# Kernel optimization log

Hardware: AMD Instinct MI355X
Metric: run time of the kernel (lower is better)

The kernel has to match this reference:

```python
import jax, jax.numpy as jnp
import numpy as np

IN_FEATURES = 1024
OUT_FEATURES = 1024
N = 8192

def setup_inputs() -> dict:
    key = jax.random.key(0)
    kx, kw, kb = jax.random.split(key, 3)
    x = jax.random.normal(kx, (N, IN_FEATURES), dtype=jnp.float32)
    # nn.Linear default init: U(-1/sqrt(in), 1/sqrt(in))
    bound = 1.0 / np.sqrt(IN_FEATURES)
    W = jax.random.uniform(kw, (OUT_FEATURES, IN_FEATURES), minval=-bound, maxval=bound, dtype=jnp.float32)
    b = jax.random.uniform(kb, (OUT_FEATURES,), minval=-bound, maxval=bound, dtype=jnp.float32)
    return {"x": x, "W": W, "b": b}

def reference(x, W, b):
    # h: [N, D]
    h = x @ W.T + b
    # scores: [N, N]; tanh applied to raw scores, softmax over dim=1 (rows)
    scores = jnp.tanh(h @ h.T)
    attn = jax.nn.softmax(scores, axis=1)
    out = jnp.tanh(attn @ h)
    return out
```

## Files before the change

kernel.cpp:

```cpp
#include <hip/hip_runtime.h>
#include <hip/hip_bf16.h>
#include <cstdint>
#include <cstddef>

typedef __bf16 bf16_t;
typedef __bf16 bf16x4 __attribute__((ext_vector_type(4)));
typedef __bf16 bf16x8 __attribute__((ext_vector_type(8)));
typedef float f32x4 __attribute__((ext_vector_type(4)));
typedef float f32x16 __attribute__((ext_vector_type(16)));
typedef float f32x2 __attribute__((ext_vector_type(2)));
typedef int i32x4 __attribute__((ext_vector_type(4)));
typedef int i32x8 __attribute__((ext_vector_type(8)));

#define NROWS 8192
#define DFEAT 1024
#define BK 32
#define NBLK 64
#define TILE_B (128 * BK)
#define F8TILE 8192
#define NTRI (NBLK * (NBLK + 1) / 2)

typedef __attribute__((address_space(3))) unsigned int lds_uint;
typedef __attribute__((address_space(1))) const unsigned int glb_uint;

__device__ __forceinline__ float fast_tanh(float x) {
  float e = __expf(2.0f * x);
  return 1.0f - 2.0f * __builtin_amdgcn_rcpf(e + 1.0f);
}

__device__ __forceinline__ unsigned pack_fp8x4(float a, float b, float c, float d) {
  unsigned v = 0;
  v = __builtin_amdgcn_cvt_pk_fp8_f32(a, b, v, false);
  v = __builtin_amdgcn_cvt_pk_fp8_f32(c, d, v, true);
  return v;
}

__global__ __launch_bounds__(256) void cast_kernel(const float* __restrict__ in,
                                                   bf16_t* __restrict__ out, int n4) {
  int i = blockIdx.x * 256 + threadIdx.x;
  if (i < n4) {
    float4 v = *(const float4*)(in + i * 4);
    bf16x4 o = {(bf16_t)v.x, (bf16_t)v.y, (bf16_t)v.z, (bf16_t)v.w};
    *(bf16x4*)(out + i * 4) = o;
  }
}

__device__ __forceinline__ void stage_async(const bf16_t* __restrict__ g, int ld,
                                            int row0, int k0, bf16_t* lds,
                                            int wave, int lane) {
#pragma unroll
  for (int t = 0; t < 2; ++t) {
    const int rb = (t * 4 + wave) * 16;
    const bf16_t* gp = g + (size_t)(row0 + rb + (lane >> 2)) * ld + (k0 + (lane & 3) * 8);
    __builtin_amdgcn_global_load_lds((glb_uint*)gp, (lds_uint*)(lds + rb * BK), 16, 0, 0);
  }
}

__device__ __forceinline__ void stage_f8(const uint8_t* __restrict__ g, int ld,
                                         int row0, int k0, uint8_t* lds,
                                         int wave, int lane) {
#pragma unroll
  for (int t = 0; t < 2; ++t) {
    const int rb = (t * 4 + wave) * 16;
    const uint8_t* gp = g + (size_t)(row0 + rb + (lane >> 2)) * ld + (k0 + (lane & 3) * 16);
    __builtin_amdgcn_global_load_lds((glb_uint*)gp, (lds_uint*)(lds + rb * 64), 16, 0, 0);
  }
}

__global__ __launch_bounds__(256) void gemm1_kernel(const bf16_t* __restrict__ xb,
                                                    const bf16_t* __restrict__ Wb,
                                                    const float* __restrict__ bias,
                                                    bf16_t* __restrict__ hout,
                                                    uint8_t* __restrict__ hT8) {
  __shared__ __align__(16) bf16_t smem[4 * TILE_B];
  const int tid = threadIdx.x;
  const int wave = tid >> 6, lane = tid & 63;
  const int wm = wave >> 1, wn = wave & 1;
  const int l15 = lane & 15, quad = lane >> 4;
  const int m0 = blockIdx.x * 128, n0 = blockIdx.y * 128;
  f32x4 acc[4][4] = {};
  const int NIT = DFEAT / BK;
  stage_async(xb, DFEAT, m0, 0, smem, wave, lane);
  stage_async(Wb, DFEAT, n0, 0, smem + TILE_B, wave, lane);
  __syncthreads();
  for (int it = 0; it < NIT; ++it) {
    bf16_t* lA = smem + (it & 1) * 2 * TILE_B;
    bf16_t* lB = lA + TILE_B;
    if (it + 1 < NIT) {
      bf16_t* nA = smem + ((it + 1) & 1) * 2 * TILE_B;
      stage_async(xb, DFEAT, m0, (it + 1) * BK, nA, wave, lane);
      stage_async(Wb, DFEAT, n0, (it + 1) * BK, nA + TILE_B, wave, lane);
    }
    bf16x8 a[4], b[4];
#pragma unroll
    for (int f = 0; f < 4; ++f) {
      a[f] = *(const bf16x8*)(lA + (wm * 64 + f * 16 + l15) * BK + quad * 8);
      b[f] = *(const bf16x8*)(lB + (wn * 64 + f * 16 + l15) * BK + quad * 8);
    }
#pragma unroll
    for (int i = 0; i < 4; ++i)
#pragma unroll
      for (int j = 0; j < 4; ++j)
        acc[i][j] = __builtin_amdgcn_mfma_f32_16x16x32_bf16(a[i], b[j], acc[i][j], 0, 0, 0);
    __syncthreads();
  }
#pragma unroll
  for (int i = 0; i < 4; ++i) {
    int rbase = m0 + wm * 64 + i * 16 + quad * 4;
#pragma unroll
    for (int j = 0; j < 4; ++j) {
      int col = n0 + wn * 64 + j * 16 + l15;
      float bv = bias[col];
      float hv[4];
#pragma unroll
      for (int r = 0; r < 4; ++r) hv[r] = acc[i][j][r] + bv;
#pragma unroll
      for (int r = 0; r < 4; ++r)
        hout[(size_t)(rbase + r) * DFEAT + col] = (bf16_t)hv[r];
      *(unsigned*)(hT8 + (size_t)col * NROWS + rbase) =
          pack_fp8x4(hv[0], hv[1], hv[2], hv[3]);
    }
  }
}

__global__ __launch_bounds__(256) void scores_sym_kernel(const bf16_t* __restrict__ h,
                                                         uint8_t* __restrict__ P,
                                                         float* __restrict__ lsum) {
  __shared__ __align__(16) char smem[128 * 144];
  bf16_t* lA = (bf16_t*)smem;
  bf16_t* lB = (bf16_t*)(smem + 128 * BK * 2);
  uint8_t (*mir)[144] = (uint8_t(*)[144])smem;

  const int k = (int)blockIdx.x & 7;
  const int s = (int)blockIdx.x >> 3;
  int I, J, r, c;
  if (s < 36) {
    I = J = k;
    int tt = s; r = 0;
    while (tt >= 8 - r) { tt -= 8 - r; ++r; }
    c = r + tt;
  } else {
    int e, t;
    if (s < 228) { e = 3 * k + (s - 36) / 64; t = (s - 36) & 63; }
    else { e = 24 + (k >> 1); t = ((k & 1) << 5) + (s - 228); }
    int ee = e; I = 0;
    while (ee >= 7 - I) { ee -= 7 - I; ++I; }
    J = I + 1 + ee;
    r = t >> 3; c = t & 7;
  }
  const int bm = I * 8 + r, bn = J * 8 + c;
  const bool offdiag = (bm != bn);
  const int m0 = bm * 128, n0 = bn * 128;

  const int tid = threadIdx.x;
  const int wave = tid >> 6, lane = tid & 63;
  const int wm = wave >> 1, wn = wave & 1;
  const int l15 = lane & 15, quad = lane >> 4;

  f32x4 acc[4][4] = {};
  for (int k0 = 0; k0 < DFEAT; k0 += BK) {
    __syncthreads();
    stage_async(h, DFEAT, m0, k0, lA, wave, lane);
    stage_async(h, DFEAT, n0, k0, lB, wave, lane);
    __syncthreads();
    bf16x8 a[4], b[4];
#pragma unroll
    for (int f = 0; f < 4; ++f) {
      a[f] = *(const bf16x8*)(lA + (wm * 64 + f * 16 + l15) * BK + quad * 8);
      b[f] = *(const bf16x8*)(lB + (wn * 64 + f * 16 + l15) * BK + quad * 8);
    }
#pragma unroll
    for (int i = 0; i < 4; ++i)
#pragma unroll
      for (int j = 0; j < 4; ++j)
        acc[i][j] = __builtin_amdgcn_mfma_f32_16x16x32_bf16(a[i], b[j], acc[i][j], 0, 0, 0);
  }
  __syncthreads();

  float rs[4][4];
  float cs[4];
#pragma unroll
  for (int i = 0; i < 4; ++i)
#pragma unroll
    for (int r2 = 0; r2 < 4; ++r2) rs[i][r2] = 0.f;
#pragma unroll
  for (int j = 0; j < 4; ++j) cs[j] = 0.f;

#pragma unroll
  for (int i = 0; i < 4; ++i) {
    const int rl_loc = wm * 64 + i * 16 + quad * 4;
    const int rbase = m0 + rl_loc;
#pragma unroll
    for (int j = 0; j < 4; ++j) {
      const int cl_loc = wn * 64 + j * 16 + l15;
      const int col = n0 + cl_loc;
      float p[4];
#pragma unroll
      for (int r2 = 0; r2 < 4; ++r2) p[r2] = __expf(fast_tanh(acc[i][j][r2]));
      unsigned packed = pack_fp8x4(p[0], p[1], p[2], p[3]);
      f32x2 d0 = __builtin_amdgcn_cvt_pk_f32_fp8(packed, false);
      f32x2 d1 = __builtin_amdgcn_cvt_pk_f32_fp8(packed, true);
      float q[4] = {d0.x, d0.y, d1.x, d1.y};
#pragma unroll
      for (int r2 = 0; r2 < 4; ++r2) {
        rs[i][r2] += q[r2];
        cs[j] += q[r2];
        P[(size_t)(rbase + r2) * NROWS + col] = (uint8_t)(packed >> (8 * r2));
      }
      if (offdiag) *(unsigned*)&mir[cl_loc][rl_loc] = packed;
    }
  }

#pragma unroll
  for (int off = 1; off < 16; off <<= 1)
#pragma unroll
    for (int i = 0; i < 4; ++i)
#pragma unroll
      for (int r2 = 0; r2 < 4; ++r2) rs[i][r2] += __shfl_xor(rs[i][r2], off, 64);
  if (l15 == 0) {
#pragma unroll
    for (int i = 0; i < 4; ++i) {
      int rbase = m0 + wm * 64 + i * 16 + quad * 4;
#pragma unroll
      for (int r2 = 0; r2 < 4; ++r2) atomicAdd(&lsum[rbase + r2], rs[i][r2]);
    }
  }

  if (offdiag) {
#pragma unroll
    for (int off = 16; off < 64; off <<= 1)
#pragma unroll
      for (int j = 0; j < 4; ++j) cs[j] += __shfl_xor(cs[j], off, 64);
    if (quad == 0) {
#pragma unroll
      for (int j = 0; j < 4; ++j)
        atomicAdd(&lsum[n0 + wn * 64 + j * 16 + l15], cs[j]);
    }
    __syncthreads();
#pragma unroll
    for (int it = 0; it < 4; ++it) {
      int q2 = tid + it * 256;
      int c2 = q2 >> 3, r0 = (q2 & 7) * 16;
      uint4 v = *(const uint4*)(&mir[c2][r0]);
      *(uint4*)(P + (size_t)(n0 + c2) * NROWS + m0 + r0) = v;
    }
  }
}

__global__ __launch_bounds__(256) void pv_kernel(const uint8_t* __restrict__ P,
                                                 const uint8_t* __restrict__ hT8,
                                                 const float* __restrict__ lsum,
                                                 float* __restrict__ out) {
  __shared__ __align__(16) uint8_t smem[4 * F8TILE];
  const int tid = threadIdx.x;
  const int wave = tid >> 6, lane = tid & 63;
  const int wm = wave >> 1, wn = wave & 1;
  const int l31 = lane & 31, khalf = lane >> 5;
  const int m0 = blockIdx.x * 128, n0 = blockIdx.y * 128;
  f32x16 acc[2][2] = {};
  const int NIT = NROWS / 64;
  stage_f8(P, NROWS, m0, 0, smem, wave, lane);
  stage_f8(hT8, NROWS, n0, 0, smem + F8TILE, wave, lane);
  __syncthreads();
  for (int it = 0; it < NIT; ++it) {
    uint8_t* lA = smem + (it & 1) * 2 * F8TILE;
    uint8_t* lB = lA + F8TILE;
    if (it + 1 < NIT) {
      uint8_t* nA = smem + ((it + 1) & 1) * 2 * F8TILE;
      stage_f8(P, NROWS, m0, (it + 1) * 64, nA, wave, lane);
      stage_f8(hT8, NROWS, n0, (it + 1) * 64, nA + F8TILE, wave, lane);
    }
    i32x8 a[2], b[2];
#pragma unroll
    for (int f = 0; f < 2; ++f) {
      {
        int off = (wm * 64 + f * 32 + l31) * 64 + khalf * 32;
        i32x4 lo = *(const i32x4*)(lA + off);
        i32x4 hi = *(const i32x4*)(lA + off + 16);
        a[f] = i32x8{lo[0], lo[1], lo[2], lo[3], hi[0], hi[1], hi[2], hi[3]};
      }
      {
        int off = (wn * 64 + f * 32 + l31) * 64 + khalf * 32;
        i32x4 lo = *(const i32x4*)(lB + off);
        i32x4 hi = *(const i32x4*)(lB + off + 16);
        b[f] = i32x8{lo[0], lo[1], lo[2], lo[3], hi[0], hi[1], hi[2], hi[3]};
      }
    }
#pragma unroll
    for (int bi = 0; bi < 2; ++bi)
#pragma unroll
      for (int bj = 0; bj < 2; ++bj)
        acc[bi][bj] = __builtin_amdgcn_mfma_scale_f32_32x32x64_f8f6f4(
            a[bi], b[bj], acc[bi][bj], 0, 0, 0, 0x7F7F7F7F, 0, 0x7F7F7F7F);
    __syncthreads();
  }
#pragma unroll
  for (int bi = 0; bi < 2; ++bi)
#pragma unroll
    for (int bj = 0; bj < 2; ++bj) {
      int cbase = n0 + wn * 64 + bj * 32 + l31;
#pragma unroll
      for (int reg = 0; reg < 16; ++reg) {
        int row = m0 + wm * 64 + bi * 32 + (reg & 3) + 8 * (reg >> 2) + 4 * khalf;
        float rl = __builtin_amdgcn_rcpf(lsum[row]);
        out[(size_t)row * DFEAT + cbase] = fast_tanh(acc[bi][bj][reg] * rl);
      }
    }
}

extern "C" void kernel_launch(void* const* d_in, const int* in_sizes, int n_in,
                              void* d_out, int out_size, void* d_ws, size_t ws_size,
                              hipStream_t stream) {
  const float* x = (const float*)d_in[0];
  const float* W = (const float*)d_in[1];
  const float* bias = (const float*)d_in[2];
  float* out = (float*)d_out;

  bf16_t* xb = (bf16_t*)d_ws;
  bf16_t* Wb = xb + (size_t)NROWS * DFEAT;
  bf16_t* h  = Wb + (size_t)DFEAT * DFEAT;
  uint8_t* hT8 = (uint8_t*)(h + (size_t)NROWS * DFEAT);
  float* lsum = (float*)(hT8 + (size_t)DFEAT * NROWS);
  uint8_t* P = (uint8_t*)(lsum + NROWS);

  cast_kernel<<<(NROWS * DFEAT / 4) / 256, 256, 0, stream>>>(x, xb, NROWS * DFEAT / 4);
  cast_kernel<<<(DFEAT * DFEAT / 4) / 256, 256, 0, stream>>>(W, Wb, DFEAT * DFEAT / 4);
  gemm1_kernel<<<dim3(NROWS / 128, DFEAT / 128), 256, 0, stream>>>(xb, Wb, bias, h, hT8);
  hipMemsetAsync(lsum, 0, NROWS * sizeof(float), stream);
  scores_sym_kernel<<<NTRI, 256, 0, stream>>>(h, P, lsum);
  pv_kernel<<<dim3(NROWS / 128, DFEAT / 128), 256, 0, stream>>>(P, hT8, lsum, out);
}
```

Baseline: 297.6 us.

## XOR-swizzle LDS staging layout and overlap next-tile loads with MFMA in scores kernel

Permutes the 16-byte column chunks in the async global-to-LDS staging with an XOR of row bits, and applies the matching permutation on the LDS fragment reads in all three GEMM kernels. The goal is to remove LDS bank conflicts on the fragment loads. The scores kernel also moves to a single-buffer prefetch: fragments are read into registers, then the next K tile's loads are issued before the MFMAs so memory latency overlaps compute. A sched_barrier keeps that ordering, at the cost of scheduling freedom.

```diff
diff --git a/kernel.cpp b/kernel.cpp
--- a/kernel.cpp
+++ b/kernel.cpp
@@ -48,10 +48,11 @@
 __device__ __forceinline__ void stage_async(const bf16_t* __restrict__ g, int ld,
                                             int row0, int k0, bf16_t* lds,
                                             int wave, int lane) {
+  const int csw = ((lane & 3) ^ ((lane >> 3) & 3)) * 8;
 #pragma unroll
   for (int t = 0; t < 2; ++t) {
     const int rb = (t * 4 + wave) * 16;
-    const bf16_t* gp = g + (size_t)(row0 + rb + (lane >> 2)) * ld + (k0 + (lane & 3) * 8);
+    const bf16_t* gp = g + (size_t)(row0 + rb + (lane >> 2)) * ld + (k0 + csw);
     __builtin_amdgcn_global_load_lds((glb_uint*)gp, (lds_uint*)(lds + rb * BK), 16, 0, 0);
   }
 }
@@ -59,10 +60,11 @@
 __device__ __forceinline__ void stage_f8(const uint8_t* __restrict__ g, int ld,
                                          int row0, int k0, uint8_t* lds,
                                          int wave, int lane) {
+  const int csw = ((lane & 3) ^ ((lane >> 3) & 3)) * 16;
 #pragma unroll
   for (int t = 0; t < 2; ++t) {
     const int rb = (t * 4 + wave) * 16;
-    const uint8_t* gp = g + (size_t)(row0 + rb + (lane >> 2)) * ld + (k0 + (lane & 3) * 16);
+    const uint8_t* gp = g + (size_t)(row0 + rb + (lane >> 2)) * ld + (k0 + csw);
     __builtin_amdgcn_global_load_lds((glb_uint*)gp, (lds_uint*)(lds + rb * 64), 16, 0, 0);
   }
 }
@@ -77,6 +79,7 @@
   const int wave = tid >> 6, lane = tid & 63;
   const int wm = wave >> 1, wn = wave & 1;
   const int l15 = lane & 15, quad = lane >> 4;
+  const int qsw = (quad ^ ((l15 >> 1) & 3)) * 8;
   const int m0 = blockIdx.x * 128, n0 = blockIdx.y * 128;
   f32x4 acc[4][4] = {};
   const int NIT = DFEAT / BK;
@@ -94,8 +97,8 @@
     bf16x8 a[4], b[4];
 #pragma unroll
     for (int f = 0; f < 4; ++f) {
-      a[f] = *(const bf16x8*)(lA + (wm * 64 + f * 16 + l15) * BK + quad * 8);
-      b[f] = *(const bf16x8*)(lB + (wn * 64 + f * 16 + l15) * BK + quad * 8);
+      a[f] = *(const bf16x8*)(lA + (wm * 64 + f * 16 + l15) * BK + qsw);
+      b[f] = *(const bf16x8*)(lB + (wn * 64 + f * 16 + l15) * BK + qsw);
     }
 #pragma unroll
     for (int i = 0; i < 4; ++i)
@@ -156,26 +159,32 @@
   const int wave = tid >> 6, lane = tid & 63;
   const int wm = wave >> 1, wn = wave & 1;
   const int l15 = lane & 15, quad = lane >> 4;
+  const int qsw = (quad ^ ((l15 >> 1) & 3)) * 8;
 
   f32x4 acc[4][4] = {};
-  for (int k0 = 0; k0 < DFEAT; k0 += BK) {
-    __syncthreads();
-    stage_async(h, DFEAT, m0, k0, lA, wave, lane);
-    stage_async(h, DFEAT, n0, k0, lB, wave, lane);
+  const int NIT = DFEAT / BK;
+  stage_async(h, DFEAT, m0, 0, lA, wave, lane);
+  stage_async(h, DFEAT, n0, 0, lB, wave, lane);
+  for (int it = 0; it < NIT; ++it) {
     __syncthreads();
     bf16x8 a[4], b[4];
 #pragma unroll
     for (int f = 0; f < 4; ++f) {
-      a[f] = *(const bf16x8*)(lA + (wm * 64 + f * 16 + l15) * BK + quad * 8);
-      b[f] = *(const bf16x8*)(lB + (wn * 64 + f * 16 + l15) * BK + quad * 8);
-    }
+      a[f] = *(const bf16x8*)(lA + (wm * 64 + f * 16 + l15) * BK + qsw);
+      b[f] = *(const bf16x8*)(lB + (wn * 64 + f * 16 + l15) * BK + qsw);
+    }
+    __syncthreads();
+    if (it + 1 < NIT) {
+      stage_async(h, DFEAT, m0, (it + 1) * BK, lA, wave, lane);
+      stage_async(h, DFEAT, n0, (it + 1) * BK, lB, wave, lane);
+    }
+    __builtin_amdgcn_sched_barrier(0);
 #pragma unroll
     for (int i = 0; i < 4; ++i)
 #pragma unroll
       for (int j = 0; j < 4; ++j)
         acc[i][j] = __builtin_amdgcn_mfma_f32_16x16x32_bf16(a[i], b[j], acc[i][j], 0, 0, 0);
   }
-  __syncthreads();
 
   float rs[4][4];
   float cs[4];
@@ -256,6 +265,7 @@
   const int wave = tid >> 6, lane = tid & 63;
   const int wm = wave >> 1, wn = wave & 1;
   const int l31 = lane & 31, khalf = lane >> 5;
+  const int s5 = (l31 >> 1) & 3;
   const int m0 = blockIdx.x * 128, n0 = blockIdx.y * 128;
   f32x16 acc[2][2] = {};
   const int NIT = NROWS / 64;
@@ -274,15 +284,15 @@
 #pragma unroll
     for (int f = 0; f < 2; ++f) {
       {
-        int off = (wm * 64 + f * 32 + l31) * 64 + khalf * 32;
-        i32x4 lo = *(const i32x4*)(lA + off);
-        i32x4 hi = *(const i32x4*)(lA + off + 16);
+        int off = (wm * 64 + f * 32 + l31) * 64;
+        i32x4 lo = *(const i32x4*)(lA + off + (((khalf * 2) ^ s5) * 16));
+        i32x4 hi = *(const i32x4*)(lA + off + (((khalf * 2 + 1) ^ s5) * 16));
         a[f] = i32x8{lo[0], lo[1], lo[2], lo[3], hi[0], hi[1], hi[2], hi[3]};
       }
       {
-        int off = (wn * 64 + f * 32 + l31) * 64 + khalf * 32;
-        i32x4 lo = *(const i32x4*)(lB + off);
-        i32x4 hi = *(const i32x4*)(lB + off + 16);
+        int off = (wn * 64 + f * 32 + l31) * 64;
+        i32x4 lo = *(const i32x4*)(lB + off + (((khalf * 2) ^ s5) * 16));
+        i32x4 hi = *(const i32x4*)(lB + off + (((khalf * 2 + 1) ^ s5) * 16));
         b[f] = i32x8{lo[0], lo[1], lo[2], lo[3], hi[0], hi[1], hi[2], hi[3]};
       }
     }
```

Result: slower. 319.8 us (+7.5%).

## Enlarge symmetric scores tiles to 256x256 with double-buffered swizzled LDS staging

Applied to the files above, without the earlier changes.

The symmetric h·hᵀ scores kernel now uses 256x256 output tiles over a 32x32 triangular block grid, with 512 threads (8 waves) per block. Each k-step is 64 wide and staged into double-buffered LDS with an XOR swizzle, so the next tile's global loads overlap the current MFMAs. The old kernel synchronised twice per k-step on 32-wide tiles. Larger tiles halve global traffic per FLOP and cut the number of blocks (528), but 128 KB of LDS and heavy register use limit occupancy to one block per CU, and a 528-block grid may underfill the GPU.

```diff
diff --git a/kernel.cpp b/kernel.cpp
--- a/kernel.cpp
+++ b/kernel.cpp
@@ -18,7 +18,8 @@
 #define NBLK 64
 #define TILE_B (128 * BK)
 #define F8TILE 8192
-#define NTRI (NBLK * (NBLK + 1) / 2)
+#define NB2 32
+#define NTRI2 528
 
 typedef __attribute__((address_space(3))) unsigned int lds_uint;
 typedef __attribute__((address_space(1))) const unsigned int glb_uint;
@@ -64,6 +65,19 @@
     const int rb = (t * 4 + wave) * 16;
     const uint8_t* gp = g + (size_t)(row0 + rb + (lane >> 2)) * ld + (k0 + (lane & 3) * 16);
     __builtin_amdgcn_global_load_lds((glb_uint*)gp, (lds_uint*)(lds + rb * 64), 16, 0, 0);
+  }
+}
+
+__device__ __forceinline__ void stage256(const bf16_t* __restrict__ g,
+                                         int row0, int kt, bf16_t* lds,
+                                         int wave, int lane) {
+  const int cg = (lane & 7) ^ ((wave * 4 + (lane >> 4)) & 7);
+#pragma unroll
+  for (int o = 0; o < 4; ++o) {
+    const int row = o * 64 + wave * 8 + (lane >> 3);
+    const bf16_t* gp = g + (size_t)(row0 + row) * DFEAT + kt * 64 + cg * 8;
+    __builtin_amdgcn_global_load_lds((glb_uint*)gp,
+        (lds_uint*)(lds + o * 4096 + wave * 512 + lane * 8), 16, 0, 0);
   }
 }
 
@@ -123,72 +137,85 @@
   }
 }
 
-__global__ __launch_bounds__(256) void scores_sym_kernel(const bf16_t* __restrict__ h,
-                                                         uint8_t* __restrict__ P,
-                                                         float* __restrict__ lsum) {
-  __shared__ __align__(16) char smem[128 * 144];
-  bf16_t* lA = (bf16_t*)smem;
-  bf16_t* lB = (bf16_t*)(smem + 128 * BK * 2);
-  uint8_t (*mir)[144] = (uint8_t(*)[144])smem;
+__global__ __launch_bounds__(512, 1) void scores_sym_kernel(const bf16_t* __restrict__ h,
+                                                            uint8_t* __restrict__ P,
+                                                            float* __restrict__ lsum) {
+  __shared__ __align__(16) char smem_raw[131072];
+  bf16_t* smb = (bf16_t*)smem_raw;
+  uint8_t (*mir)[272] = (uint8_t(*)[272])smem_raw;
 
   const int k = (int)blockIdx.x & 7;
   const int s = (int)blockIdx.x >> 3;
   int I, J, r, c;
-  if (s < 36) {
+  if (s < 10) {
     I = J = k;
     int tt = s; r = 0;
-    while (tt >= 8 - r) { tt -= 8 - r; ++r; }
+    while (tt >= 4 - r) { tt -= 4 - r; ++r; }
     c = r + tt;
   } else {
     int e, t;
-    if (s < 228) { e = 3 * k + (s - 36) / 64; t = (s - 36) & 63; }
-    else { e = 24 + (k >> 1); t = ((k & 1) << 5) + (s - 228); }
+    if (s < 58) { e = 3 * k + (s - 10) / 16; t = (s - 10) & 15; }
+    else { e = 24 + (k >> 1); t = ((k & 1) << 3) + (s - 58); }
     int ee = e; I = 0;
     while (ee >= 7 - I) { ee -= 7 - I; ++I; }
     J = I + 1 + ee;
-    r = t >> 3; c = t & 7;
-  }
-  const int bm = I * 8 + r, bn = J * 8 + c;
+    r = t >> 2; c = t & 3;
+  }
+  const int bm = I * 4 + r, bn = J * 4 + c;
   const bool offdiag = (bm != bn);
-  const int m0 = bm * 128, n0 = bn * 128;
+  const int m0 = bm * 256, n0 = bn * 256;
 
   const int tid = threadIdx.x;
   const int wave = tid >> 6, lane = tid & 63;
-  const int wm = wave >> 1, wn = wave & 1;
+  const int wm = wave >> 2, wn = wave & 3;
   const int l15 = lane & 15, quad = lane >> 4;
-
-  f32x4 acc[4][4] = {};
-  for (int k0 = 0; k0 < DFEAT; k0 += BK) {
+  const int rkey = (l15 >> 1) & 7;
+
+  f32x4 acc[8][4] = {};
+  const int NKT = DFEAT / 64;
+
+  stage256(h, m0, 0, smb, wave, lane);
+  stage256(h, n0, 0, smb + 16384, wave, lane);
+  __syncthreads();
+  for (int kt = 0; kt < NKT; ++kt) {
+    bf16_t* bufA = smb + (kt & 1) * 32768;
+    bf16_t* bufB = bufA + 16384;
+    if (kt + 1 < NKT) {
+      bf16_t* nA = smb + ((kt + 1) & 1) * 32768;
+      stage256(h, m0, kt + 1, nA, wave, lane);
+      stage256(h, n0, kt + 1, nA + 16384, wave, lane);
+    }
+#pragma unroll
+    for (int ks = 0; ks < 2; ++ks) {
+      const int cp = ((ks * 4 + quad) ^ rkey) * 8;
+      bf16x8 a[8], b[4];
+#pragma unroll
+      for (int mf = 0; mf < 8; ++mf)
+        a[mf] = *(const bf16x8*)(bufA + (wm * 128 + mf * 16 + l15) * 64 + cp);
+#pragma unroll
+      for (int nf = 0; nf < 4; ++nf)
+        b[nf] = *(const bf16x8*)(bufB + (wn * 64 + nf * 16 + l15) * 64 + cp);
+#pragma unroll
+      for (int mf = 0; mf < 8; ++mf)
+#pragma unroll
+        for (int nf = 0; nf < 4; ++nf)
+          acc[mf][nf] = __builtin_amdgcn_mfma_f32_16x16x32_bf16(a[mf], b[nf], acc[mf][nf], 0, 0, 0);
+    }
     __syncthreads();
-    stage_async(h, DFEAT, m0, k0, lA, wave, lane);
-    stage_async(h, DFEAT, n0, k0, lB, wave, lane);
-    __syncthreads();
-    bf16x8 a[4], b[4];
-#pragma unroll
-    for (int f = 0; f < 4; ++f) {
-      a[f] = *(const bf16x8*)(lA + (wm * 64 + f * 16 + l15) * BK + quad * 8);
-      b[f] = *(const bf16x8*)(lB + (wn * 64 + f * 16 + l15) * BK + quad * 8);
-    }
-#pragma unroll
-    for (int i = 0; i < 4; ++i)
-#pragma unroll
-      for (int j = 0; j < 4; ++j)
-        acc[i][j] = __builtin_amdgcn_mfma_f32_16x16x32_bf16(a[i], b[j], acc[i][j], 0, 0, 0);
-  }
-  __syncthreads();
-
-  float rs[4][4];
+  }
+
+  float rs[8][4];
   float cs[4];
 #pragma unroll
-  for (int i = 0; i < 4; ++i)
+  for (int i = 0; i < 8; ++i)
 #pragma unroll
     for (int r2 = 0; r2 < 4; ++r2) rs[i][r2] = 0.f;
 #pragma unroll
   for (int j = 0; j < 4; ++j) cs[j] = 0.f;
 
 #pragma unroll
-  for (int i = 0; i < 4; ++i) {
-    const int rl_loc = wm * 64 + i * 16 + quad * 4;
+  for (int i = 0; i < 8; ++i) {
+    const int rl_loc = wm * 128 + i * 16 + quad * 4;
     const int rbase = m0 + rl_loc;
 #pragma unroll
     for (int j = 0; j < 4; ++j) {
@@ -214,13 +241,13 @@
 #pragma unroll
   for (int off = 1; off < 16; off <<= 1)
 #pragma unroll
-    for (int i = 0; i < 4; ++i)
+    for (int i = 0; i < 8; ++i)
 #pragma unroll
       for (int r2 = 0; r2 < 4; ++r2) rs[i][r2] += __shfl_xor(rs[i][r2], off, 64);
   if (l15 == 0) {
 #pragma unroll
-    for (int i = 0; i < 4; ++i) {
-      int rbase = m0 + wm * 64 + i * 16 + quad * 4;
+    for (int i = 0; i < 8; ++i) {
+      int rbase = m0 + wm * 128 + i * 16 + quad * 4;
 #pragma unroll
       for (int r2 = 0; r2 < 4; ++r2) atomicAdd(&lsum[rbase + r2], rs[i][r2]);
     }
@@ -238,9 +265,9 @@
     }
     __syncthreads();
 #pragma unroll
-    for (int it = 0; it < 4; ++it) {
-      int q2 = tid + it * 256;
-      int c2 = q2 >> 3, r0 = (q2 & 7) * 16;
+    for (int it = 0; it < 8; ++it) {
+      int q2 = tid + it * 512;
+      int c2 = q2 >> 4, r0 = (q2 & 15) * 16;
       uint4 v = *(const uint4*)(&mir[c2][r0]);
       *(uint4*)(P + (size_t)(n0 + c2) * NROWS + m0 + r0) = v;
     }
@@ -327,6 +354,6 @@
   cast_kernel<<<(DFEAT * DFEAT / 4) / 256, 256, 0, stream>>>(W, Wb, DFEAT * DFEAT / 4);
   gemm1_kernel<<<dim3(NROWS / 128, DFEAT / 128), 256, 0, stream>>>(xb, Wb, bias, h, hT8);
   hipMemsetAsync(lsum, 0, NROWS * sizeof(float), stream);
-  scores_sym_kernel<<<NTRI, 256, 0, stream>>>(h, P, lsum);
+  scores_sym_kernel<<<NTRI2, 512, 0, stream>>>(h, P, lsum);
   pv_kernel<<<dim3(NROWS / 128, DFEAT / 128), 256, 0, stream>>>(P, hT8, lsum, out);
 }
```

Result: slower. 314.7 us (+5.8%).
